# Optimization experiments

Measured on AMD Instinct MI355X. Metric: run time of the kernel, lower is better.

## Reference

```python
import jax, jax.numpy as jnp
import numpy as np
import math

B, L, D, H = 2, 2048, 512, 8
DH = D // H  # 64
MAX_SEQ = 2048


def setup_inputs() -> dict:
    key = jax.random.key(0)
    ks = jax.random.split(key, 9)
    rn = lambda k, sh: jax.random.normal(k, sh, dtype=jnp.float32)
    w_scale = 0.02
    # causal mask: 1 where attention is disallowed (upper triangle)
    causal = jnp.triu(jnp.ones((L, L), jnp.float32), k=1)[None, None]
    return {
        "q_in": rn(ks[0], (B, L, D)),
        "k_in": rn(ks[1], (B, L, D)),
        "v_in": rn(ks[2], (B, L, D)),
        "mask": causal,
        "Wq": rn(ks[3], (D, D)) * w_scale,
        "bq": jnp.zeros((D,), jnp.float32),
        "Wk": rn(ks[4], (D, D)) * w_scale,
        "bk": jnp.zeros((D,), jnp.float32),
        "Wv": rn(ks[5], (D, D)) * w_scale,
        "bv": jnp.zeros((D,), jnp.float32),
        "Wfc": rn(ks[6], (D, D)) * w_scale,
        "bfc": jnp.zeros((D,), jnp.float32),
        "E": rn(ks[7], (MAX_SEQ, DH)),  # relative position embedding (non-trainable buffer)
    }


def _heads(x, W, b):
    # [B,L,D] -> [B,H,L,DH]
    y = x @ W + b
    return y.reshape(x.shape[0], x.shape[1], H, DH).transpose(0, 2, 1, 3)


def _qe_mask(len_q):
    # keep[l, m] = (m >= len_q - 1 - l); zeros out invalid relative offsets
    rows = jnp.arange(len_q)[:, None]
    cols = jnp.arange(len_q)[None, :]
    return (cols >= (len_q - 1 - rows)).astype(jnp.float32)


def _skew(QE):
    # Music-Transformer skewing: [B,H,L,M] -> pad left on last dim ->
    # reshape swapping last two dims -> drop first row => Srel [B,H,M,L]
    b, h, l, m = QE.shape
    padded = jnp.pad(QE, ((0, 0), (0, 0), (0, 0), (1, 0)))  # [b,h,l,m+1]
    reshaped = padded.reshape(b, h, m + 1, l)
    return reshaped[:, :, 1:, :]  # [b,h,m,l]


def reference(q_in, k_in, v_in, mask, Wq, bq, Wk, bk, Wv, bv, Wfc, bfc, E):
    q = _heads(q_in, Wq, bq)  # [B,H,L,DH]
    k = _heads(k_in, Wk, bk)
    v = _heads(v_in, Wv, bv)
    len_q = q.shape[2]
    # left embedding slice: E[max(0, MAX_SEQ - len_q):]
    e = E[max(0, MAX_SEQ - len_q):, :]  # [M, DH], M == len_q here
    QE = jnp.einsum('bhld,md->bhlm', q, e)
    QE = QE * _qe_mask(len_q)  # broadcast [L,M] over [B,H,L,M]
    Srel = _skew(QE)  # [B,H,L,L]
    QKt = jnp.einsum('bhld,bhmd->bhlm', q, k)
    logits = (QKt + Srel) / np.sqrt(DH).astype(np.float32)
    logits = logits + mask * (-1e9)
    attn_weights = jax.nn.softmax(logits, axis=-1)
    attn = jnp.einsum('bhlm,bhmd->bhld', attn_weights, v)
    out = attn.transpose(0, 2, 1, 3).reshape(q_in.shape[0], -1, D)
    out = out @ Wfc + bfc
    return out, attn_weights
```

## Files before the change

kernel.cpp:

```cpp
#include <hip/hip_runtime.h>
#include <math.h>

#define L 2048
#define DMODEL 512
#define NH 8
#define DH 64
#define NROWS 4096

typedef __attribute__((ext_vector_type(4))) float f32x4;
typedef __attribute__((ext_vector_type(8))) short s16x8;

#define MFMA(a, b, c) __builtin_amdgcn_mfma_f32_16x16x32_bf16(a, b, c, 0, 0, 0)

static __device__ __forceinline__ ushort f2b(float f) {
    union { float f; unsigned u; } v; v.f = f;
    unsigned r = v.u + 0x7FFF + ((v.u >> 16) & 1);
    return (ushort)(r >> 16);
}
static __device__ __forceinline__ float b2f(ushort u) {
    union { unsigned u; float f; } v; v.u = ((unsigned)u) << 16;
    return v.f;
}

__global__ __launch_bounds__(256)
void cvt_bf16(const float* __restrict__ in, ushort* __restrict__ out, int n8) {
    int i = blockIdx.x * 256 + threadIdx.x;
    if (i < n8) {
        float4 a = *reinterpret_cast<const float4*>(&in[(size_t)i * 8]);
        float4 b = *reinterpret_cast<const float4*>(&in[(size_t)i * 8 + 4]);
        ushort4 o0; o0.x = f2b(a.x); o0.y = f2b(a.y); o0.z = f2b(a.z); o0.w = f2b(a.w);
        ushort4 o1; o1.x = f2b(b.x); o1.y = f2b(b.y); o1.z = f2b(b.z); o1.w = f2b(b.w);
        *reinterpret_cast<ushort4*>(&out[(size_t)i * 8]) = o0;
        *reinterpret_cast<ushort4*>(&out[(size_t)i * 8 + 4]) = o1;
    }
}

__global__ __launch_bounds__(256)
void transpose_w(const float* __restrict__ W0, const float* __restrict__ W1,
                 const float* __restrict__ W2, const float* __restrict__ W3,
                 ushort* __restrict__ T0, ushort* __restrict__ T1,
                 ushort* __restrict__ T2, ushort* __restrict__ T3) {
    const int z = blockIdx.z;
    const float* W = z == 0 ? W0 : (z == 1 ? W1 : (z == 2 ? W2 : W3));
    ushort* T = z == 0 ? T0 : (z == 1 ? T1 : (z == 2 ? T2 : T3));
    __shared__ float Ls[64][65];
    const int tid = threadIdx.x;
    const int k0 = blockIdx.y * 64, n0 = blockIdx.x * 64;
    #pragma unroll
    for (int i = 0; i < 4; ++i) {
        int kk = (tid >> 4) + i * 16, n4 = (tid & 15) * 4;
        float4 v = *reinterpret_cast<const float4*>(&W[(size_t)(k0 + kk) * 512 + n0 + n4]);
        Ls[kk][n4] = v.x; Ls[kk][n4 + 1] = v.y; Ls[kk][n4 + 2] = v.z; Ls[kk][n4 + 3] = v.w;
    }
    __syncthreads();
    #pragma unroll
    for (int i = 0; i < 4; ++i) {
        int nn = (tid >> 4) + i * 16, k4 = (tid & 15) * 4;
        ushort4 o;
        o.x = f2b(Ls[k4 + 0][nn]); o.y = f2b(Ls[k4 + 1][nn]);
        o.z = f2b(Ls[k4 + 2][nn]); o.w = f2b(Ls[k4 + 3][nn]);
        *reinterpret_cast<ushort4*>(&T[(size_t)(n0 + nn) * 512 + k0 + k4]) = o;
    }
}

__global__ __launch_bounds__(256)
void gemm_bf16(const void* __restrict__ A0, const void* __restrict__ A1,
               const void* __restrict__ A2,
               const ushort* __restrict__ W0, const ushort* __restrict__ W1,
               const ushort* __restrict__ W2,
               const float* __restrict__ b0, const float* __restrict__ b1,
               const float* __restrict__ b2,
               void* o0, void* o1, void* o2, int a_f32, int mode) {
    const int z = blockIdx.z;
    const void* A   = z == 0 ? A0 : (z == 1 ? A1 : A2);
    const ushort* Wt = z == 0 ? W0 : (z == 1 ? W1 : W2);
    const float* bias = z == 0 ? b0 : (z == 1 ? b1 : b2);
    void* outp = z == 0 ? o0 : (z == 1 ? o1 : o2);

    __shared__ ushort As[128][40];
    __shared__ ushort Bs[64][40];
    const int tid = threadIdx.x;
    const int w = tid >> 6, lane = tid & 63, g = lane >> 4, c = lane & 15;
    const int m0 = blockIdx.y * 128, n0 = blockIdx.x * 64;

    f32x4 acc[2][4];
    #pragma unroll
    for (int rs = 0; rs < 2; ++rs)
        #pragma unroll
        for (int cs = 0; cs < 4; ++cs) acc[rs][cs] = (f32x4){0.f, 0.f, 0.f, 0.f};

    float bsv[4];
    #pragma unroll
    for (int cs = 0; cs < 4; ++cs) bsv[cs] = bias[n0 + 16 * cs + c];

    for (int k0 = 0; k0 < 512; k0 += 32) {
        {
            int row = tid >> 1, kh = (tid & 1) * 16;
            if (a_f32) {
                const float* p = (const float*)A + (size_t)(m0 + row) * 512 + k0 + kh;
                ushort tmp[16];
                #pragma unroll
                for (int q4 = 0; q4 < 4; ++q4) {
                    float4 f = *reinterpret_cast<const float4*>(p + q4 * 4);
                    tmp[q4 * 4 + 0] = f2b(f.x); tmp[q4 * 4 + 1] = f2b(f.y);
                    tmp[q4 * 4 + 2] = f2b(f.z); tmp[q4 * 4 + 3] = f2b(f.w);
                }
                *reinterpret_cast<uint4*>(&As[row][kh]) = *reinterpret_cast<uint4*>(&tmp[0]);
                *reinterpret_cast<uint4*>(&As[row][kh + 8]) = *reinterpret_cast<uint4*>(&tmp[8]);
            } else {
                const ushort* p = (const ushort*)A + (size_t)(m0 + row) * 512 + k0 + kh;
                uint4 x0 = *reinterpret_cast<const uint4*>(p);
                uint4 x1 = *reinterpret_cast<const uint4*>(p + 8);
                *reinterpret_cast<uint4*>(&As[row][kh]) = x0;
                *reinterpret_cast<uint4*>(&As[row][kh + 8]) = x1;
            }
        }
        {
            int n = tid >> 2, kh = (tid & 3) * 8;
            uint4 x = *reinterpret_cast<const uint4*>(&Wt[(size_t)(n0 + n) * 512 + k0 + kh]);
            *reinterpret_cast<uint4*>(&Bs[n][kh]) = x;
        }
        __syncthreads();
        s16x8 af[2], bf[4];
        #pragma unroll
        for (int rs = 0; rs < 2; ++rs)
            af[rs] = *reinterpret_cast<const s16x8*>(&As[32 * w + 16 * rs + c][8 * g]);
        #pragma unroll
        for (int cs = 0; cs < 4; ++cs)
            bf[cs] = *reinterpret_cast<const s16x8*>(&Bs[16 * cs + c][8 * g]);
        #pragma unroll
        for (int rs = 0; rs < 2; ++rs)
            #pragma unroll
            for (int cs = 0; cs < 4; ++cs)
                acc[rs][cs] = MFMA(af[rs], bf[cs], acc[rs][cs]);
        __syncthreads();
    }
    #pragma unroll
    for (int rs = 0; rs < 2; ++rs)
        #pragma unroll
        for (int cs = 0; cs < 4; ++cs)
            #pragma unroll
            for (int r = 0; r < 4; ++r) {
                int row = m0 + 32 * w + 16 * rs + 4 * g + r;
                int n = n0 + 16 * cs + c;
                float v = acc[rs][cs][r] + bsv[cs];
                if (mode == 0) {
                    ((float*)outp)[(size_t)row * 512 + n] = v;
                } else {
                    int bb = row >> 11, l = row & 2047, hh = n >> 6, dh = n & 63;
                    ((ushort*)outp)[(((size_t)bb * NH + hh) * L + l) * DH + dh] = f2b(v);
                }
            }
}

__global__ __launch_bounds__(256, 3)
void attn(const ushort* __restrict__ qws, const ushort* __restrict__ kws,
          const ushort* __restrict__ vws, const ushort* __restrict__ Ebf,
          float* __restrict__ attnw, ushort* __restrict__ ows) {
    __shared__ float  Tst[2][32][100];
    __shared__ ushort Vt[2][64][68];
    __shared__ ushort Ptile[2][32][68];
    __shared__ float  redm[4][32], reds[4][32];
    __shared__ float  mrow[32], linv[32];

    const int tid = threadIdx.x;
    const int w = tid >> 6, lane = tid & 63, g = lane >> 4, c = lane & 15;
    const int bid = blockIdx.x;
    const int bh = bid & 15;
    const int ib = 63 - (bid >> 4);
    const int b = bh >> 3, h = bh & 7;
    const int i0 = ib * 32;
    const int nj = (ib >> 1) + 1;

    const ushort* qb = qws + (size_t)bh * L * DH;
    const ushort* kb = kws + (size_t)bh * L * DH;
    const ushort* vb = vws + (size_t)bh * L * DH;
    float* ab = attnw + (size_t)bh * L * L;

    s16x8 aq[2][2];
    #pragma unroll
    for (int rs = 0; rs < 2; ++rs)
        #pragma unroll
        for (int ks = 0; ks < 2; ++ks)
            aq[rs][ks] = *reinterpret_cast<const s16x8*>(
                qb + (size_t)(i0 + 16 * rs + c) * DH + 32 * ks + 8 * g);

    auto computeS = [&](int j0, int buf, float (&sv)[2][4], int doV,
                        const uint4& vv0, const uint4& vv1) {
        const int rbase = L - 32 - i0 + j0;
        const int ncts = (w < 2) ? 2 : 1;
        f32x4 TT[2][2];
        for (int cti = 0; cti < ncts; ++cti) {
            int ct = w + cti * 4;
            s16x8 be[2];
            #pragma unroll
            for (int ks = 0; ks < 2; ++ks) {
                int rg = rbase + 16 * ct + c;
                rg = rg < 0 ? 0 : (rg > L - 1 ? L - 1 : rg);
                be[ks] = *reinterpret_cast<const s16x8*>(
                    Ebf + (size_t)rg * DH + 32 * ks + 8 * g);
            }
            #pragma unroll
            for (int rs = 0; rs < 2; ++rs) {
                f32x4 t = {0.f, 0.f, 0.f, 0.f};
                t = MFMA(aq[rs][0], be[0], t);
                t = MFMA(aq[rs][1], be[1], t);
                TT[cti][rs] = t;
            }
        }
        f32x4 SK[2];
        {
            s16x8 bk[2];
            #pragma unroll
            for (int ks = 0; ks < 2; ++ks)
                bk[ks] = *reinterpret_cast<const s16x8*>(
                    kb + (size_t)(j0 + 16 * w + c) * DH + 32 * ks + 8 * g);
            #pragma unroll
            for (int rs = 0; rs < 2; ++rs) {
                f32x4 t = {0.f, 0.f, 0.f, 0.f};
                t = MFMA(aq[rs][0], bk[0], t);
                t = MFMA(aq[rs][1], bk[1], t);
                SK[rs] = t;
            }
        }
        for (int cti = 0; cti < ncts; ++cti) {
            int ct = w + cti * 4;
            #pragma unroll
            for (int rs = 0; rs < 2; ++rs)
                #pragma unroll
                for (int r = 0; r < 4; ++r)
                    Tst[buf][16 * rs + 4 * g + r][16 * ct + c] = TT[cti][rs][r];
        }
        if (doV) {
            const int jj = tid >> 2, d8 = (tid & 3) * 16;
            const ushort* pv = (const ushort*)&vv0;
            #pragma unroll
            for (int e = 0; e < 8; ++e) Vt[buf][d8 + e][jj] = pv[e];
            pv = (const ushort*)&vv1;
            #pragma unroll
            for (int e = 0; e < 8; ++e) Vt[buf][d8 + 8 + e][jj] = pv[e];
        }
        __syncthreads();
        #pragma unroll
        for (int rs = 0; rs < 2; ++rs)
            #pragma unroll
            for (int r = 0; r < 4; ++r) {
                int il = 16 * rs + 4 * g + r;
                int jl = 16 * w + c;
                float s = (SK[rs][r] + Tst[buf][il][31 + jl - il]) * 0.125f;
                sv[rs][r] = (j0 + jl <= i0 + il) ? s : -1.0e30f;
            }
    };

    float mw[2][4], lw[2][4];
    #pragma unroll
    for (int rs = 0; rs < 2; ++rs)
        #pragma unroll
        for (int r = 0; r < 4; ++r) { mw[rs][r] = -1.0e30f; lw[rs][r] = 0.f; }
    uint4 zu = {0, 0, 0, 0};
    for (int tj = 0; tj < nj; ++tj) {
        float sv[2][4];
        computeS(tj * 64, tj & 1, sv, 0, zu, zu);
        #pragma unroll
        for (int rs = 0; rs < 2; ++rs)
            #pragma unroll
            for (int r = 0; r < 4; ++r) {
                float s = sv[rs][r];
                float mn = fmaxf(mw[rs][r], s);
                lw[rs][r] = lw[rs][r] * __expf(mw[rs][r] - mn) + __expf(s - mn);
                mw[rs][r] = mn;
            }
    }
    #pragma unroll
    for (int rs = 0; rs < 2; ++rs)
        #pragma unroll
        for (int r = 0; r < 4; ++r) {
            float m = mw[rs][r], l = lw[rs][r];
            #pragma unroll
            for (int d = 1; d < 16; d <<= 1) {
                float om = __shfl_xor(m, d);
                float ol = __shfl_xor(l, d);
                float mn = fmaxf(m, om);
                l = l * __expf(m - mn) + ol * __expf(om - mn);
                m = mn;
            }
            if (c == 0) {
                int il = 16 * rs + 4 * g + r;
                redm[w][il] = m;
                reds[w][il] = l;
            }
        }
    __syncthreads();
    if (tid < 32) {
        float m0 = redm[0][tid], m1 = redm[1][tid];
        float m2 = redm[2][tid], m3 = redm[3][tid];
        float m = fmaxf(fmaxf(m0, m1), fmaxf(m2, m3));
        float l = reds[0][tid] * __expf(m0 - m) + reds[1][tid] * __expf(m1 - m)
                + reds[2][tid] * __expf(m2 - m) + reds[3][tid] * __expf(m3 - m);
        mrow[tid] = m;
        linv[tid] = 1.0f / l;
    }
    __syncthreads();
    float mym[2][4], myi[2][4];
    #pragma unroll
    for (int rs = 0; rs < 2; ++rs)
        #pragma unroll
        for (int r = 0; r < 4; ++r) {
            int il = 16 * rs + 4 * g + r;
            mym[rs][r] = mrow[il];
            myi[rs][r] = linv[il];
        }

    f32x4 O0 = {0.f, 0.f, 0.f, 0.f}, O1 = {0.f, 0.f, 0.f, 0.f};
    for (int tj = 0; tj < nj; ++tj) {
        const int j0 = tj * 64;
        const int buf = tj & 1;
        uint4 vv0, vv1;
        {
            const int jj = tid >> 2, d8 = (tid & 3) * 16;
            const ushort* vp = vb + (size_t)(j0 + jj) * DH + d8;
            vv0 = *reinterpret_cast<const uint4*>(vp);
            vv1 = *reinterpret_cast<const uint4*>(vp + 8);
        }
        float sv[2][4];
        computeS(j0, buf, sv, 1, vv0, vv1);
        #pragma unroll
        for (int rs = 0; rs < 2; ++rs)
            #pragma unroll
            for (int r = 0; r < 4; ++r) {
                int il = 16 * rs + 4 * g + r;
                float p = __expf(sv[rs][r] - mym[rs][r]) * myi[rs][r];
                Ptile[buf][il][16 * w + c] = f2b(p);
            }
        __syncthreads();
        {
            const int row = tid >> 3, c8 = (tid & 7) * 8;
            ushort4 u0 = *reinterpret_cast<const ushort4*>(&Ptile[buf][row][c8]);
            ushort4 u1 = *reinterpret_cast<const ushort4*>(&Ptile[buf][row][c8 + 4]);
            float4 f0 = make_float4(b2f(u0.x), b2f(u0.y), b2f(u0.z), b2f(u0.w));
            float4 f1 = make_float4(b2f(u1.x), b2f(u1.y), b2f(u1.z), b2f(u1.w));
            float* dst = &ab[(size_t)(i0 + row) * L + j0 + c8];
            *reinterpret_cast<float4*>(dst) = f0;
            *reinterpret_cast<float4*>(dst + 4) = f1;
        }
        #pragma unroll
        for (int ks = 0; ks < 2; ++ks) {
            s16x8 bv = *reinterpret_cast<const s16x8*>(&Vt[buf][16 * w + c][32 * ks + 8 * g]);
            s16x8 pa0 = *reinterpret_cast<const s16x8*>(&Ptile[buf][c][32 * ks + 8 * g]);
            s16x8 pa1 = *reinterpret_cast<const s16x8*>(&Ptile[buf][16 + c][32 * ks + 8 * g]);
            O0 = MFMA(pa0, bv, O0);
            O1 = MFMA(pa1, bv, O1);
        }
    }

    {
        const int row = tid >> 3, c8 = (tid & 7) * 8;
        const float4 z = make_float4(0.f, 0.f, 0.f, 0.f);
        for (int j0 = nj * 64; j0 < L; j0 += 64) {
            float* dst = &ab[(size_t)(i0 + row) * L + j0 + c8];
            *reinterpret_cast<float4*>(dst) = z;
            *reinterpret_cast<float4*>(dst + 4) = z;
        }
    }

    #pragma unroll
    for (int rs = 0; rs < 2; ++rs)
        #pragma unroll
        for (int r = 0; r < 4; ++r) {
            int il = 16 * rs + 4 * g + r;
            float v = (rs ? O1[r] : O0[r]);
            ows[((size_t)b * L + i0 + il) * DMODEL + h * DH + 16 * w + c] = f2b(v);
        }
}

extern "C" void kernel_launch(void* const* d_in, const int* in_sizes, int n_in,
                              void* d_out, int out_size, void* d_ws, size_t ws_size,
                              hipStream_t stream) {
    const float* q_in = (const float*)d_in[0];
    const float* k_in = (const float*)d_in[1];
    const float* v_in = (const float*)d_in[2];
    const float* Wq  = (const float*)d_in[4];
    const float* bq  = (const float*)d_in[5];
    const float* Wk  = (const float*)d_in[6];
    const float* bk  = (const float*)d_in[7];
    const float* Wv  = (const float*)d_in[8];
    const float* bv  = (const float*)d_in[9];
    const float* Wfc = (const float*)d_in[10];
    const float* bfc = (const float*)d_in[11];
    const float* E   = (const float*)d_in[12];

    float* out0  = (float*)d_out;
    float* attnw = out0 + (size_t)2 * L * DMODEL;

    const size_t NA = (size_t)NROWS * DMODEL;
    ushort* ws = (ushort*)d_ws;
    ushort* Ebf  = ws;
    ushort* Wqt  = Ebf + (size_t)L * DH;
    ushort* Wkt  = Wqt + 262144;
    ushort* Wvt  = Wkt + 262144;
    ushort* Wfct = Wvt + 262144;
    ushort* qws  = Wfct + 262144;
    ushort* kws  = qws + NA;
    ushort* vws  = kws + NA;
    ushort* ows  = vws + NA;

    cvt_bf16<<<dim3(64), 256, 0, stream>>>(E, Ebf, (int)(L * DH / 8));
    transpose_w<<<dim3(8, 8, 4), 256, 0, stream>>>(Wq, Wk, Wv, Wfc, Wqt, Wkt, Wvt, Wfct);
    gemm_bf16<<<dim3(8, 32, 3), 256, 0, stream>>>(q_in, k_in, v_in, Wqt, Wkt, Wvt,
                                                  bq, bk, bv, qws, kws, vws, 1, 1);
    attn<<<dim3(1024), 256, 0, stream>>>(qws, kws, vws, Ebf, attnw, ows);
    gemm_bf16<<<dim3(8, 32, 1), 256, 0, stream>>>(ows, ows, ows, Wfct, Wfct, Wfct,
                                                  bfc, bfc, bfc, out0, out0, out0, 0, 0);
}
```

Before: 240.6 us.

## Make attention single-pass and move normalization into a separate rescale kernel

The two-pass online-softmax attention, which recomputed the scores twice, becomes a single pass. Each pass now accumulates exp(s) without subtracting the row max, builds the relative-position skew with lane shuffles instead of shared memory, and gives each warp its own key tiles and P·V accumulators, which are reduced across warps at the end. V is written pre-transposed by the projection GEMM, so V fragments load directly from global memory. A new rescale kernel multiplies the stored unnormalized weights by 1/rowsum and zero-fills the masked region. In exchange, the attention matrix is read and written an extra time, and dropping the max subtraction risks overflow for large logits.

```diff
diff --git a/kernel.cpp b/kernel.cpp
--- a/kernel.cpp
+++ b/kernel.cpp
@@ -16,10 +16,6 @@
     union { float f; unsigned u; } v; v.f = f;
     unsigned r = v.u + 0x7FFF + ((v.u >> 16) & 1);
     return (ushort)(r >> 16);
-}
-static __device__ __forceinline__ float b2f(ushort u) {
-    union { unsigned u; float f; } v; v.u = ((unsigned)u) << 16;
-    return v.f;
 }
 
 __global__ __launch_bounds__(256)
@@ -65,17 +61,14 @@
 
 __global__ __launch_bounds__(256)
 void gemm_bf16(const void* __restrict__ A0, const void* __restrict__ A1,
-               const void* __restrict__ A2,
                const ushort* __restrict__ W0, const ushort* __restrict__ W1,
-               const ushort* __restrict__ W2,
                const float* __restrict__ b0, const float* __restrict__ b1,
-               const float* __restrict__ b2,
-               void* o0, void* o1, void* o2, int a_f32, int mode) {
+               void* o0, void* o1, int a_f32, int mode) {
     const int z = blockIdx.z;
-    const void* A   = z == 0 ? A0 : (z == 1 ? A1 : A2);
-    const ushort* Wt = z == 0 ? W0 : (z == 1 ? W1 : W2);
-    const float* bias = z == 0 ? b0 : (z == 1 ? b1 : b2);
-    void* outp = z == 0 ? o0 : (z == 1 ? o1 : o2);
+    const void* A   = z == 0 ? A0 : A1;
+    const ushort* Wt = z == 0 ? W0 : W1;
+    const float* bias = z == 0 ? b0 : b1;
+    void* outp = z == 0 ? o0 : o1;
 
     __shared__ ushort As[128][40];
     __shared__ ushort Bs[64][40];
@@ -144,24 +137,25 @@
                 int row = m0 + 32 * w + 16 * rs + 4 * g + r;
                 int n = n0 + 16 * cs + c;
                 float v = acc[rs][cs][r] + bsv[cs];
+                int bb = row >> 11, l = row & 2047, hh = n >> 6, dh = n & 63;
                 if (mode == 0) {
                     ((float*)outp)[(size_t)row * 512 + n] = v;
+                } else if (mode == 1) {
+                    ((ushort*)outp)[(((size_t)bb * NH + hh) * L + l) * DH + dh] = f2b(v);
                 } else {
-                    int bb = row >> 11, l = row & 2047, hh = n >> 6, dh = n & 63;
-                    ((ushort*)outp)[(((size_t)bb * NH + hh) * L + l) * DH + dh] = f2b(v);
+                    ((ushort*)outp)[(((size_t)bb * NH + hh) * DH + dh) * L + l] = f2b(v);
                 }
             }
 }
 
 __global__ __launch_bounds__(256, 3)
 void attn(const ushort* __restrict__ qws, const ushort* __restrict__ kws,
-          const ushort* __restrict__ vws, const ushort* __restrict__ Ebf,
-          float* __restrict__ attnw, ushort* __restrict__ ows) {
-    __shared__ float  Tst[2][32][100];
-    __shared__ ushort Vt[2][64][68];
-    __shared__ ushort Ptile[2][32][68];
-    __shared__ float  redm[4][32], reds[4][32];
-    __shared__ float  mrow[32], linv[32];
+          const ushort* __restrict__ vtg, const ushort* __restrict__ Ebf,
+          float* __restrict__ attnw, ushort* __restrict__ ows,
+          float* __restrict__ linvg) {
+    __shared__ float Ored[4][32][68];
+    __shared__ float lred[4][32];
+    __shared__ float linvs[32];
 
     const int tid = threadIdx.x;
     const int w = tid >> 6, lane = tid & 63, g = lane >> 4, c = lane & 15;
@@ -170,12 +164,14 @@
     const int ib = 63 - (bid >> 4);
     const int b = bh >> 3, h = bh & 7;
     const int i0 = ib * 32;
-    const int nj = (ib >> 1) + 1;
+    const int nt = ib + 1;
 
     const ushort* qb = qws + (size_t)bh * L * DH;
     const ushort* kb = kws + (size_t)bh * L * DH;
-    const ushort* vb = vws + (size_t)bh * L * DH;
+    const ushort* vt = vtg + (size_t)bh * DH * L;
     float* ab = attnw + (size_t)bh * L * L;
+
+    ushort (*Pw)[40] = reinterpret_cast<ushort(*)[40]>(&Ored[w][0][0]);
 
     s16x8 aq[2][2];
     #pragma unroll
@@ -185,192 +181,163 @@
             aq[rs][ks] = *reinterpret_cast<const s16x8*>(
                 qb + (size_t)(i0 + 16 * rs + c) * DH + 32 * ks + 8 * g);
 
-    auto computeS = [&](int j0, int buf, float (&sv)[2][4], int doV,
-                        const uint4& vv0, const uint4& vv1) {
+    f32x4 O[2][4];
+    #pragma unroll
+    for (int rs = 0; rs < 2; ++rs)
+        #pragma unroll
+        for (int cs = 0; cs < 4; ++cs) O[rs][cs] = (f32x4){0.f, 0.f, 0.f, 0.f};
+    float lsum[2][4] = {};
+
+    for (int t = w; t < nt; t += 4) {
+        const int j0 = t * 32;
         const int rbase = L - 32 - i0 + j0;
-        const int ncts = (w < 2) ? 2 : 1;
-        f32x4 TT[2][2];
-        for (int cti = 0; cti < ncts; ++cti) {
-            int ct = w + cti * 4;
+
+        f32x4 TT[4][2];
+        #pragma unroll
+        for (int ct = 0; ct < 4; ++ct) {
             s16x8 be[2];
-            #pragma unroll
-            for (int ks = 0; ks < 2; ++ks) {
-                int rg = rbase + 16 * ct + c;
-                rg = rg < 0 ? 0 : (rg > L - 1 ? L - 1 : rg);
+            int rg = rbase + 16 * ct + c;
+            rg = rg > L - 1 ? L - 1 : rg;
+            #pragma unroll
+            for (int ks = 0; ks < 2; ++ks)
                 be[ks] = *reinterpret_cast<const s16x8*>(
                     Ebf + (size_t)rg * DH + 32 * ks + 8 * g);
+            #pragma unroll
+            for (int rs = 0; rs < 2; ++rs) {
+                f32x4 x = {0.f, 0.f, 0.f, 0.f};
+                x = MFMA(aq[rs][0], be[0], x);
+                x = MFMA(aq[rs][1], be[1], x);
+                TT[ct][rs] = x;
             }
-            #pragma unroll
-            for (int rs = 0; rs < 2; ++rs) {
-                f32x4 t = {0.f, 0.f, 0.f, 0.f};
-                t = MFMA(aq[rs][0], be[0], t);
-                t = MFMA(aq[rs][1], be[1], t);
-                TT[cti][rs] = t;
-            }
-        }
-        f32x4 SK[2];
+        }
+        float rel[2][2][4];
+        #pragma unroll
+        for (int r = 0; r < 4; ++r) {
+            const int u = c - 4 * g - r;
+            const int src = (lane & 48) | ((15 + u) & 15);
+            const bool hi = (u >= 1);
+            #pragma unroll
+            for (int rs = 0; rs < 2; ++rs)
+                #pragma unroll
+                for (int jh = 0; jh < 2; ++jh) {
+                    const int b0 = jh - rs + 1;
+                    float va = __shfl(TT[b0][rs][r], src);
+                    float vb = __shfl(TT[b0 + 1][rs][r], src);
+                    rel[rs][jh][r] = hi ? vb : va;
+                }
+        }
+        f32x4 SK[2][2];
         {
-            s16x8 bk[2];
-            #pragma unroll
-            for (int ks = 0; ks < 2; ++ks)
-                bk[ks] = *reinterpret_cast<const s16x8*>(
-                    kb + (size_t)(j0 + 16 * w + c) * DH + 32 * ks + 8 * g);
-            #pragma unroll
-            for (int rs = 0; rs < 2; ++rs) {
-                f32x4 t = {0.f, 0.f, 0.f, 0.f};
-                t = MFMA(aq[rs][0], bk[0], t);
-                t = MFMA(aq[rs][1], bk[1], t);
-                SK[rs] = t;
-            }
-        }
-        for (int cti = 0; cti < ncts; ++cti) {
-            int ct = w + cti * 4;
+            s16x8 bk[2][2];
+            #pragma unroll
+            for (int jh = 0; jh < 2; ++jh)
+                #pragma unroll
+                for (int ks = 0; ks < 2; ++ks)
+                    bk[jh][ks] = *reinterpret_cast<const s16x8*>(
+                        kb + (size_t)(j0 + 16 * jh + c) * DH + 32 * ks + 8 * g);
             #pragma unroll
             for (int rs = 0; rs < 2; ++rs)
                 #pragma unroll
-                for (int r = 0; r < 4; ++r)
-                    Tst[buf][16 * rs + 4 * g + r][16 * ct + c] = TT[cti][rs][r];
-        }
-        if (doV) {
-            const int jj = tid >> 2, d8 = (tid & 3) * 16;
-            const ushort* pv = (const ushort*)&vv0;
-            #pragma unroll
-            for (int e = 0; e < 8; ++e) Vt[buf][d8 + e][jj] = pv[e];
-            pv = (const ushort*)&vv1;
-            #pragma unroll
-            for (int e = 0; e < 8; ++e) Vt[buf][d8 + 8 + e][jj] = pv[e];
-        }
-        __syncthreads();
+                for (int jh = 0; jh < 2; ++jh) {
+                    f32x4 x = {0.f, 0.f, 0.f, 0.f};
+                    x = MFMA(aq[rs][0], bk[jh][0], x);
+                    x = MFMA(aq[rs][1], bk[jh][1], x);
+                    SK[rs][jh] = x;
+                }
+        }
         #pragma unroll
         for (int rs = 0; rs < 2; ++rs)
             #pragma unroll
-            for (int r = 0; r < 4; ++r) {
-                int il = 16 * rs + 4 * g + r;
-                int jl = 16 * w + c;
-                float s = (SK[rs][r] + Tst[buf][il][31 + jl - il]) * 0.125f;
-                sv[rs][r] = (j0 + jl <= i0 + il) ? s : -1.0e30f;
-            }
-    };
-
-    float mw[2][4], lw[2][4];
-    #pragma unroll
-    for (int rs = 0; rs < 2; ++rs)
-        #pragma unroll
-        for (int r = 0; r < 4; ++r) { mw[rs][r] = -1.0e30f; lw[rs][r] = 0.f; }
-    uint4 zu = {0, 0, 0, 0};
-    for (int tj = 0; tj < nj; ++tj) {
-        float sv[2][4];
-        computeS(tj * 64, tj & 1, sv, 0, zu, zu);
-        #pragma unroll
-        for (int rs = 0; rs < 2; ++rs)
-            #pragma unroll
-            for (int r = 0; r < 4; ++r) {
-                float s = sv[rs][r];
-                float mn = fmaxf(mw[rs][r], s);
-                lw[rs][r] = lw[rs][r] * __expf(mw[rs][r] - mn) + __expf(s - mn);
-                mw[rs][r] = mn;
-            }
-    }
+            for (int jh = 0; jh < 2; ++jh)
+                #pragma unroll
+                for (int r = 0; r < 4; ++r) {
+                    const int il = 16 * rs + 4 * g + r;
+                    const int jl = 16 * jh + c;
+                    float s = (SK[rs][jh][r] + rel[rs][jh][r]) * 0.125f;
+                    float p = (j0 + jl <= i0 + il) ? __expf(s) : 0.0f;
+                    lsum[rs][r] += p;
+                    ab[(size_t)(i0 + il) * L + j0 + jl] = p;
+                    Pw[il][jl] = f2b(p);
+                }
+        s16x8 pa[2];
+        #pragma unroll
+        for (int rs2 = 0; rs2 < 2; ++rs2)
+            pa[rs2] = *reinterpret_cast<const s16x8*>(&Pw[16 * rs2 + c][8 * g]);
+        #pragma unroll
+        for (int cs = 0; cs < 4; ++cs) {
+            s16x8 vtb = *reinterpret_cast<const s16x8*>(
+                vt + (size_t)(16 * cs + c) * L + j0 + 8 * g);
+            #pragma unroll
+            for (int rs2 = 0; rs2 < 2; ++rs2)
+                O[rs2][cs] = MFMA(pa[rs2], vtb, O[rs2][cs]);
+        }
+    }
+
     #pragma unroll
     for (int rs = 0; rs < 2; ++rs)
         #pragma unroll
         for (int r = 0; r < 4; ++r) {
-            float m = mw[rs][r], l = lw[rs][r];
-            #pragma unroll
-            for (int d = 1; d < 16; d <<= 1) {
-                float om = __shfl_xor(m, d);
-                float ol = __shfl_xor(l, d);
-                float mn = fmaxf(m, om);
-                l = l * __expf(m - mn) + ol * __expf(om - mn);
-                m = mn;
-            }
-            if (c == 0) {
-                int il = 16 * rs + 4 * g + r;
-                redm[w][il] = m;
-                reds[w][il] = l;
-            }
-        }
+            float s = lsum[rs][r];
+            s += __shfl_xor(s, 1); s += __shfl_xor(s, 2);
+            s += __shfl_xor(s, 4); s += __shfl_xor(s, 8);
+            if (c == 0) lred[w][16 * rs + 4 * g + r] = s;
+        }
+    #pragma unroll
+    for (int rs2 = 0; rs2 < 2; ++rs2)
+        #pragma unroll
+        for (int cs = 0; cs < 4; ++cs)
+            #pragma unroll
+            for (int r = 0; r < 4; ++r)
+                Ored[w][16 * rs2 + 4 * g + r][16 * cs + c] = O[rs2][cs][r];
     __syncthreads();
     if (tid < 32) {
-        float m0 = redm[0][tid], m1 = redm[1][tid];
-        float m2 = redm[2][tid], m3 = redm[3][tid];
-        float m = fmaxf(fmaxf(m0, m1), fmaxf(m2, m3));
-        float l = reds[0][tid] * __expf(m0 - m) + reds[1][tid] * __expf(m1 - m)
-                + reds[2][tid] * __expf(m2 - m) + reds[3][tid] * __expf(m3 - m);
-        mrow[tid] = m;
-        linv[tid] = 1.0f / l;
+        float l = lred[0][tid] + lred[1][tid] + lred[2][tid] + lred[3][tid];
+        float inv = 1.0f / l;
+        linvs[tid] = inv;
+        linvg[(size_t)bh * L + i0 + tid] = inv;
     }
     __syncthreads();
-    float mym[2][4], myi[2][4];
-    #pragma unroll
-    for (int rs = 0; rs < 2; ++rs)
-        #pragma unroll
-        for (int r = 0; r < 4; ++r) {
-            int il = 16 * rs + 4 * g + r;
-            mym[rs][r] = mrow[il];
-            myi[rs][r] = linv[il];
-        }
-
-    f32x4 O0 = {0.f, 0.f, 0.f, 0.f}, O1 = {0.f, 0.f, 0.f, 0.f};
-    for (int tj = 0; tj < nj; ++tj) {
-        const int j0 = tj * 64;
-        const int buf = tj & 1;
-        uint4 vv0, vv1;
-        {
-            const int jj = tid >> 2, d8 = (tid & 3) * 16;
-            const ushort* vp = vb + (size_t)(j0 + jj) * DH + d8;
-            vv0 = *reinterpret_cast<const uint4*>(vp);
-            vv1 = *reinterpret_cast<const uint4*>(vp + 8);
-        }
-        float sv[2][4];
-        computeS(j0, buf, sv, 1, vv0, vv1);
-        #pragma unroll
-        for (int rs = 0; rs < 2; ++rs)
-            #pragma unroll
-            for (int r = 0; r < 4; ++r) {
-                int il = 16 * rs + 4 * g + r;
-                float p = __expf(sv[rs][r] - mym[rs][r]) * myi[rs][r];
-                Ptile[buf][il][16 * w + c] = f2b(p);
-            }
-        __syncthreads();
-        {
-            const int row = tid >> 3, c8 = (tid & 7) * 8;
-            ushort4 u0 = *reinterpret_cast<const ushort4*>(&Ptile[buf][row][c8]);
-            ushort4 u1 = *reinterpret_cast<const ushort4*>(&Ptile[buf][row][c8 + 4]);
-            float4 f0 = make_float4(b2f(u0.x), b2f(u0.y), b2f(u0.z), b2f(u0.w));
-            float4 f1 = make_float4(b2f(u1.x), b2f(u1.y), b2f(u1.z), b2f(u1.w));
-            float* dst = &ab[(size_t)(i0 + row) * L + j0 + c8];
-            *reinterpret_cast<float4*>(dst) = f0;
-            *reinterpret_cast<float4*>(dst + 4) = f1;
-        }
-        #pragma unroll
-        for (int ks = 0; ks < 2; ++ks) {
-            s16x8 bv = *reinterpret_cast<const s16x8*>(&Vt[buf][16 * w + c][32 * ks + 8 * g]);
-            s16x8 pa0 = *reinterpret_cast<const s16x8*>(&Ptile[buf][c][32 * ks + 8 * g]);
-            s16x8 pa1 = *reinterpret_cast<const s16x8*>(&Ptile[buf][16 + c][32 * ks + 8 * g]);
-            O0 = MFMA(pa0, bv, O0);
-            O1 = MFMA(pa1, bv, O1);
-        }
-    }
-
     {
-        const int row = tid >> 3, c8 = (tid & 7) * 8;
-        const float4 z = make_float4(0.f, 0.f, 0.f, 0.f);
-        for (int j0 = nj * 64; j0 < L; j0 += 64) {
-            float* dst = &ab[(size_t)(i0 + row) * L + j0 + c8];
-            *reinterpret_cast<float4*>(dst) = z;
-            *reinterpret_cast<float4*>(dst + 4) = z;
-        }
-    }
-
-    #pragma unroll
-    for (int rs = 0; rs < 2; ++rs)
-        #pragma unroll
-        for (int r = 0; r < 4; ++r) {
-            int il = 16 * rs + 4 * g + r;
-            float v = (rs ? O1[r] : O0[r]);
-            ows[((size_t)b * L + i0 + il) * DMODEL + h * DH + 16 * w + c] = f2b(v);
-        }
+        const int i = tid >> 3, d8 = (tid & 7) * 8;
+        const float inv = linvs[i];
+        ushort o[8];
+        #pragma unroll
+        for (int e = 0; e < 8; ++e) {
+            float a = Ored[0][i][d8 + e] + Ored[1][i][d8 + e]
+                    + Ored[2][i][d8 + e] + Ored[3][i][d8 + e];
+            o[e] = f2b(a * inv);
+        }
+        *reinterpret_cast<uint4*>(
+            &ows[((size_t)b * L + i0 + i) * DMODEL + h * DH + d8]) =
+            *reinterpret_cast<const uint4*>(&o[0]);
+    }
+}
+
+__global__ __launch_bounds__(256)
+void rescale(float* __restrict__ attnw, const float* __restrict__ linvg) {
+    const int blk = blockIdx.x;
+    const int bh = blk >> 11, i = blk & 2047;
+    const float inv = linvg[(size_t)bh * L + i];
+    float* rowp = attnw + ((size_t)bh * L + i) * L;
+    const int c8 = threadIdx.x * 8;
+    float4 a, b2;
+    if (c8 <= i) {
+        a  = *reinterpret_cast<const float4*>(rowp + c8);
+        b2 = *reinterpret_cast<const float4*>(rowp + c8 + 4);
+        a.x  = (c8 + 0 <= i) ? a.x  * inv : 0.f;
+        a.y  = (c8 + 1 <= i) ? a.y  * inv : 0.f;
+        a.z  = (c8 + 2 <= i) ? a.z  * inv : 0.f;
+        a.w  = (c8 + 3 <= i) ? a.w  * inv : 0.f;
+        b2.x = (c8 + 4 <= i) ? b2.x * inv : 0.f;
+        b2.y = (c8 + 5 <= i) ? b2.y * inv : 0.f;
+        b2.z = (c8 + 6 <= i) ? b2.z * inv : 0.f;
+        b2.w = (c8 + 7 <= i) ? b2.w * inv : 0.f;
+    } else {
+        a = make_float4(0.f, 0.f, 0.f, 0.f);
+        b2 = a;
+    }
+    *reinterpret_cast<float4*>(rowp + c8) = a;
+    *reinterpret_cast<float4*>(rowp + c8 + 4) = b2;
 }
 
 extern "C" void kernel_launch(void* const* d_in, const int* in_sizes, int n_in,
@@ -401,14 +368,18 @@
     ushort* Wfct = Wvt + 262144;
     ushort* qws  = Wfct + 262144;
     ushort* kws  = qws + NA;
-    ushort* vws  = kws + NA;
-    ushort* ows  = vws + NA;
+    ushort* vtg  = kws + NA;
+    ushort* ows  = vtg + NA;
+    float*  linvg = (float*)(ows + NA);
 
     cvt_bf16<<<dim3(64), 256, 0, stream>>>(E, Ebf, (int)(L * DH / 8));
     transpose_w<<<dim3(8, 8, 4), 256, 0, stream>>>(Wq, Wk, Wv, Wfc, Wqt, Wkt, Wvt, Wfct);
-    gemm_bf16<<<dim3(8, 32, 3), 256, 0, stream>>>(q_in, k_in, v_in, Wqt, Wkt, Wvt,
-                                                  bq, bk, bv, qws, kws, vws, 1, 1);
-    attn<<<dim3(1024), 256, 0, stream>>>(qws, kws, vws, Ebf, attnw, ows);
-    gemm_bf16<<<dim3(8, 32, 1), 256, 0, stream>>>(ows, ows, ows, Wfct, Wfct, Wfct,
-                                                  bfc, bfc, bfc, out0, out0, out0, 0, 0);
-}
+    gemm_bf16<<<dim3(8, 32, 2), 256, 0, stream>>>(q_in, k_in, Wqt, Wkt,
+                                                  bq, bk, qws, kws, 1, 1);
+    gemm_bf16<<<dim3(8, 32, 1), 256, 0, stream>>>(v_in, v_in, Wvt, Wvt,
+                                                  bv, bv, vtg, vtg, 1, 2);
+    attn<<<dim3(1024), 256, 0, stream>>>(qws, kws, vtg, Ebf, attnw, ows, linvg);
+    rescale<<<dim3(32768), 256, 0, stream>>>(attnw, linvg);
+    gemm_bf16<<<dim3(8, 32, 1), 256, 0, stream>>>(ows, ows, Wfct, Wfct,
+                                                  bfc, bfc, out0, out0, 0, 0);
+}
```

Result: faster. 216.1 us (-10.2%).
